# Kernel optimization log

Hardware: AMD Instinct MI355X
Metric: run time of the kernel (lower is better)

## Reference

```python
import jax, jax.numpy as jnp
import numpy as np

DIM = 4096
N_HEADS = 32
N_KV_HEADS = 8
HEAD_DIM = 128
B, S = 2, 2048


def setup_inputs() -> dict:
    key = jax.random.key(0)
    k1, k2, k3, k4, k5 = jax.random.split(key, 5)
    sc = 0.02
    return {
        "x": jax.random.normal(k1, (B, S, DIM), dtype=jnp.float32),
        "wq": jax.random.normal(k2, (N_HEADS * HEAD_DIM, DIM), dtype=jnp.float32) * sc,
        "wk": jax.random.normal(k3, (N_KV_HEADS * HEAD_DIM, DIM), dtype=jnp.float32) * sc,
        "wv": jax.random.normal(k4, (N_KV_HEADS * HEAD_DIM, DIM), dtype=jnp.float32) * sc,
        "wo": jax.random.normal(k5, (DIM, N_HEADS * HEAD_DIM), dtype=jnp.float32) * sc,
    }


def reference(x, wq, wk, wv, wo):
    b, s, _ = x.shape
    groups = N_HEADS // N_KV_HEADS
    # projections (torch Linear: y = x @ W.T)
    q = (x @ wq.T).reshape(b, s, N_HEADS, HEAD_DIM).transpose(0, 2, 1, 3)      # [b,H,s,d]
    k = (x @ wk.T).reshape(b, s, N_KV_HEADS, HEAD_DIM).transpose(0, 2, 1, 3)   # [b,Hkv,s,d]
    v = (x @ wv.T).reshape(b, s, N_KV_HEADS, HEAD_DIM).transpose(0, 2, 1, 3)
    # GQA: attend q grouped per kv head without materializing expanded k/v
    qg = q.reshape(b, N_KV_HEADS, groups, s, HEAD_DIM)                          # [b,Hkv,g,s,d]
    scores = jnp.einsum("bhgqd,bhkd->bhgqk", qg, k) * (HEAD_DIM ** -0.5)
    attn = jax.nn.softmax(scores, axis=-1)                                      # no causal mask (as in source)
    out = jnp.einsum("bhgqk,bhkd->bhgqd", attn, v)                              # [b,Hkv,g,s,d]
    out = out.reshape(b, N_HEADS, s, HEAD_DIM).transpose(0, 2, 1, 3).reshape(b, s, N_HEADS * HEAD_DIM)
    return out @ wo.T
```

## Files before the change

kernel.cpp:

```cpp
#include <hip/hip_runtime.h>
#include <stdint.h>


typedef __attribute__((ext_vector_type(4))) float f32x4;
typedef __attribute__((ext_vector_type(16))) float f32x16;
typedef __attribute__((ext_vector_type(4))) float float4v;
typedef __attribute__((ext_vector_type(8))) short short8;
typedef __attribute__((ext_vector_type(8))) __bf16 bf16x8;
typedef __attribute__((ext_vector_type(4))) unsigned short ushort4v;
typedef __attribute__((ext_vector_type(4))) unsigned int uint4v;

#define B_SZ 2
#define S_SZ 2048
#define DIM_SZ 4096
#define NH 32
#define NKV 8
#define HD 128
#define CEXP 0.12752531f

static __device__ __forceinline__ unsigned short f2bf(float f) {
  unsigned int u = __builtin_bit_cast(unsigned int, f);
  u = (u + 0x7fffu + ((u >> 16) & 1u)) >> 16;
  return (unsigned short)u;
}
static __device__ __forceinline__ f32x4 mfma16(short8 a, short8 b, f32x4 c) {
  return __builtin_amdgcn_mfma_f32_16x16x32_bf16(
      __builtin_bit_cast(bf16x8, a), __builtin_bit_cast(bf16x8, b), c, 0, 0, 0);
}
static __device__ __forceinline__ f32x16 mfma32(short8 a, short8 b, f32x16 c) {
  return __builtin_amdgcn_mfma_f32_32x32x16_bf16(
      __builtin_bit_cast(bf16x8, a), __builtin_bit_cast(bf16x8, b), c, 0, 0, 0);
}
static __device__ __forceinline__ void gload16(const void* g, void* l) {
  __builtin_amdgcn_global_load_lds(
      (const __attribute__((address_space(1))) unsigned int*)g,
      (__attribute__((address_space(3))) unsigned int*)l, 16, 0, 0);
}
static __device__ __forceinline__ unsigned int cvtpk(float lo, float hi) {
  unsigned int r;
  asm("v_cvt_pk_bf16_f32 %0, %1, %2" : "=v"(r) : "v"(lo), "v"(hi));
  return r;
}

__global__ __launch_bounds__(256) void cvt_kernel(const float* __restrict__ src,
                                                  unsigned short* __restrict__ dst,
                                                  int n4) {
  int i = blockIdx.x * 256 + threadIdx.x;
  if (i >= n4) return;
  float4v v = ((const float4v*)src)[i];
  ushort4v o;
  o[0] = f2bf(v[0]); o[1] = f2bf(v[1]); o[2] = f2bf(v[2]); o[3] = f2bf(v[3]);
  ((ushort4v*)dst)[i] = o;
}

template <int EPI>
__global__ __launch_bounds__(512, 2) void gemm256(const unsigned short* __restrict__ A,
                                                  const unsigned short* __restrict__ B,
                                                  void* __restrict__ Cout,
                                                  int N, int K, int H) {
  __shared__ unsigned short lds[65536];
  const int tid = threadIdx.x;
  const int lane = tid & 63;
  const int wave = tid >> 6;
  const int wm = wave >> 2;
  const int wn = wave & 3;
  const int fr = lane & 15, fg = lane >> 4;
  const int m0 = blockIdx.y * 256, n0 = blockIdx.x * 256;
  const int NT = K >> 6;

  auto seg = [&](int buf, int ab, int half) -> unsigned short* {
    return lds + ((((buf << 1) | ab) << 1) | half) * 8192;
  };

  const int srow = tid >> 3;
  const int scol = ((tid & 7) ^ (srow & 7)) << 3;
  const unsigned short* Abase = A + (size_t)(m0 + srow) * K + scol;
  const unsigned short* Bbase = B + (size_t)(n0 + srow) * K + scol;

  auto stageA = [&](int t, int h) {
    const unsigned short* g = Abase + (size_t)(h * 128) * K + t * 64;
    unsigned short* d = seg(t & 1, 0, h);
    gload16(g, d + tid * 8);
    gload16(g + (size_t)64 * K, d + 4096 + tid * 8);
  };
  auto stageB = [&](int t, int h) {
    const unsigned short* g = Bbase + (size_t)(h * 128) * K + t * 64;
    unsigned short* d = seg(t & 1, 1, h);
    gload16(g, d + tid * 8);
    gload16(g + (size_t)64 * K, d + 4096 + tid * 8);
  };

  f32x4 acc[8][4] = {};

  stageA(0, 0); stageA(0, 1);
  stageB(0, 0); stageB(0, 1);
  stageB(1, 0); stageB(1, 1);
  asm volatile("s_waitcnt vmcnt(4)" ::: "memory");
  __builtin_amdgcn_s_barrier();

#pragma unroll 1
  for (int t = 0; t < NT; ++t) {
    const unsigned short* Aseg = seg(t & 1, 0, wm);
    const unsigned short* Bseg = seg(t & 1, 1, wn >> 1);
    const int brow0 = (wn & 1) * 64;
    short8 aR[4][2], b01[2][2], b23[2][2];

#pragma unroll
    for (int mi = 0; mi < 4; ++mi)
#pragma unroll
      for (int ks = 0; ks < 2; ++ks) {
        const int row = mi * 16 + fr;
        aR[mi][ks] = *(const short8*)&Aseg[row * 64 + ((((ks << 2) + fg) ^ (row & 7)) << 3)];
      }
#pragma unroll
    for (int ni = 0; ni < 2; ++ni)
#pragma unroll
      for (int ks = 0; ks < 2; ++ks) {
        const int row = brow0 + ni * 16 + fr;
        b01[ni][ks] = *(const short8*)&Bseg[row * 64 + ((((ks << 2) + fg) ^ (row & 7)) << 3)];
      }
    if (t + 1 < NT) stageA(t + 1, 0);
    __builtin_amdgcn_sched_barrier(0);
    __builtin_amdgcn_s_barrier();
    asm volatile("s_waitcnt lgkmcnt(0)" ::: "memory");
    __builtin_amdgcn_sched_barrier(0);
    __builtin_amdgcn_s_setprio(1);
#pragma unroll
    for (int mi = 0; mi < 4; ++mi)
#pragma unroll
      for (int ni = 0; ni < 2; ++ni)
#pragma unroll
        for (int ks = 0; ks < 2; ++ks)
          acc[mi][ni] = mfma16(aR[mi][ks], b01[ni][ks], acc[mi][ni]);
    __builtin_amdgcn_s_setprio(0);
    __builtin_amdgcn_sched_barrier(0);
    __builtin_amdgcn_s_barrier();

#pragma unroll
    for (int ni = 0; ni < 2; ++ni)
#pragma unroll
      for (int ks = 0; ks < 2; ++ks) {
        const int row = brow0 + (ni + 2) * 16 + fr;
        b23[ni][ks] = *(const short8*)&Bseg[row * 64 + ((((ks << 2) + fg) ^ (row & 7)) << 3)];
      }
    if (t + 1 < NT) stageA(t + 1, 1);
    __builtin_amdgcn_sched_barrier(0);
    __builtin_amdgcn_s_barrier();
    asm volatile("s_waitcnt lgkmcnt(0)" ::: "memory");
    __builtin_amdgcn_sched_barrier(0);
    __builtin_amdgcn_s_setprio(1);
#pragma unroll
    for (int mi = 0; mi < 4; ++mi)
#pragma unroll
      for (int ni = 0; ni < 2; ++ni)
#pragma unroll
        for (int ks = 0; ks < 2; ++ks)
          acc[mi][ni + 2] = mfma16(aR[mi][ks], b23[ni][ks], acc[mi][ni + 2]);
    __builtin_amdgcn_s_setprio(0);
    __builtin_amdgcn_sched_barrier(0);
    __builtin_amdgcn_s_barrier();

#pragma unroll
    for (int mi = 0; mi < 4; ++mi)
#pragma unroll
      for (int ks = 0; ks < 2; ++ks) {
        const int row = (mi + 4) * 16 + fr;
        aR[mi][ks] = *(const short8*)&Aseg[row * 64 + ((((ks << 2) + fg) ^ (row & 7)) << 3)];
      }
    if (t + 2 < NT) stageB(t + 2, 0);
    __builtin_amdgcn_sched_barrier(0);
    __builtin_amdgcn_s_barrier();
    asm volatile("s_waitcnt lgkmcnt(0)" ::: "memory");
    __builtin_amdgcn_sched_barrier(0);
    __builtin_amdgcn_s_setprio(1);
#pragma unroll
    for (int mi = 0; mi < 4; ++mi)
#pragma unroll
      for (int ni = 0; ni < 2; ++ni)
#pragma unroll
        for (int ks = 0; ks < 2; ++ks)
          acc[mi + 4][ni] = mfma16(aR[mi][ks], b01[ni][ks], acc[mi + 4][ni]);
    __builtin_amdgcn_s_setprio(0);
    __builtin_amdgcn_sched_barrier(0);
    __builtin_amdgcn_s_barrier();

    if (t + 2 < NT) {
      stageB(t + 2, 1);
      __builtin_amdgcn_sched_barrier(0);
      asm volatile("s_waitcnt vmcnt(4)" ::: "memory");
    } else {
      __builtin_amdgcn_sched_barrier(0);
      asm volatile("s_waitcnt vmcnt(0)" ::: "memory");
    }
    __builtin_amdgcn_s_barrier();
    __builtin_amdgcn_s_setprio(1);
#pragma unroll
    for (int mi = 0; mi < 4; ++mi)
#pragma unroll
      for (int ni = 0; ni < 2; ++ni)
#pragma unroll
        for (int ks = 0; ks < 2; ++ks)
          acc[mi + 4][ni + 2] = mfma16(aR[mi][ks], b23[ni][ks], acc[mi + 4][ni + 2]);
    __builtin_amdgcn_s_setprio(0);
    __builtin_amdgcn_sched_barrier(0);
    __builtin_amdgcn_s_barrier();
  }

#pragma unroll
  for (int mi = 0; mi < 8; ++mi) {
#pragma unroll
    for (int ni = 0; ni < 4; ++ni) {
      const int mb = m0 + wm * 128 + mi * 16 + fg * 4;
      const int n = n0 + wn * 64 + ni * 16 + fr;
      if (EPI == 0) {
        float* C = (float*)Cout;
#pragma unroll
        for (int r = 0; r < 4; ++r) C[(size_t)(mb + r) * N + n] = acc[mi][ni][r];
      } else {
        unsigned short* C = (unsigned short*)Cout;
        const int h = n >> 7, d = n & 127;
#pragma unroll
        for (int r = 0; r < 4; ++r) {
          const int m = mb + r;
          const int bb = m >> 11, s = m & 2047;
          C[(((size_t)(bb * H + h)) * S_SZ + s) * HD + d] = f2bf(acc[mi][ni][r]);
        }
      }
    }
  }
}

template <int EPI>
__global__ __launch_bounds__(256) void gemm_bt(const unsigned short* __restrict__ A,
                                               const unsigned short* __restrict__ B,
                                               void* __restrict__ Cout,
                                               void* __restrict__ Cout2,
                                               int N, int K, int H) {
  __shared__ unsigned short As[128 * 32];
  __shared__ unsigned short Bs[128 * 32];
  const int tid = threadIdx.x;
  const int lane = tid & 63;
  const int wave = tid >> 6;
  const int wr = wave >> 1, wc = wave & 1;
  const int m0 = blockIdx.y * 128, n0 = blockIdx.x * 128;

  f32x4 acc[4][4] = {};

  const int srow = tid >> 2;
  const int swz8 = ((tid & 3) ^ (srow & 3)) * 8;
  const unsigned short* Ap0 = A + (size_t)(m0 + srow) * K + swz8;
  const unsigned short* Ap1 = Ap0 + (size_t)64 * K;
  const unsigned short* Bp0 = B + (size_t)(n0 + srow) * K + swz8;
  const unsigned short* Bp1 = Bp0 + (size_t)64 * K;
  unsigned short* Ad0 = As + tid * 8;
  unsigned short* Ad1 = As + 2048 + tid * 8;
  unsigned short* Bd0 = Bs + tid * 8;
  unsigned short* Bd1 = Bs + 2048 + tid * 8;

  const int fr = lane & 15;
  const int fg = lane >> 4;
  const int rsl = (fg ^ (fr & 3)) * 8;

#pragma unroll 1
  for (int kt = 0; kt < K; kt += 32) {
    gload16(Ap0 + kt, Ad0);
    gload16(Ap1 + kt, Ad1);
    gload16(Bp0 + kt, Bd0);
    gload16(Bp1 + kt, Bd1);
    __syncthreads();
    short8 a[4], b[4];
#pragma unroll
    for (int i = 0; i < 4; i++)
      a[i] = *(const short8*)&As[(wr * 64 + i * 16 + fr) * 32 + rsl];
#pragma unroll
    for (int i = 0; i < 4; i++)
      b[i] = *(const short8*)&Bs[(wc * 64 + i * 16 + fr) * 32 + rsl];
#pragma unroll
    for (int mi = 0; mi < 4; mi++)
#pragma unroll
      for (int ni = 0; ni < 4; ni++)
        acc[mi][ni] = mfma16(a[mi], b[ni], acc[mi][ni]);
    __syncthreads();
  }

#pragma unroll
  for (int mi = 0; mi < 4; mi++) {
#pragma unroll
    for (int ni = 0; ni < 4; ni++) {
      const int mb = m0 + wr * 64 + mi * 16 + fg * 4;
      const int n = n0 + wc * 64 + ni * 16 + fr;
      if (EPI == 0) {
        float* C = (float*)Cout;
#pragma unroll
        for (int r = 0; r < 4; r++) C[(size_t)(mb + r) * N + n] = acc[mi][ni][r];
      } else if (EPI == 3) {
        if (n < 1024) {
          unsigned short* C = (unsigned short*)Cout;
          const int h = n >> 7, d = n & 127;
#pragma unroll
          for (int r = 0; r < 4; r++) {
            const int m = mb + r;
            const int bb = m >> 11, s = m & 2047;
            C[(((size_t)(bb * NKV + h)) * S_SZ + s) * HD + d] = f2bf(acc[mi][ni][r]);
          }
        } else {
          unsigned short* C = (unsigned short*)Cout2;
          const int vr = n - 1024;
          const int h = vr >> 7, d = vr & 127;
          const int bb = mb >> 11, s = mb & 2047;
          ushort4v pk;
#pragma unroll
          for (int r = 0; r < 4; r++) pk[r] = f2bf(acc[mi][ni][r]);
          *(ushort4v*)&C[(((size_t)(bb * NKV + h)) * HD + d) * S_SZ + s] = pk;
        }
      }
    }
  }
}

__global__ __launch_bounds__(512) void attn_kernel(const unsigned short* __restrict__ Q,
                                                   const unsigned short* __restrict__ Kg,
                                                   const unsigned short* __restrict__ Vt,
                                                   unsigned short* __restrict__ AO) {
  __shared__ unsigned short Ks[2][64 * 128];
  __shared__ unsigned short Vs[2][128 * 64];
  const int tid = threadIdx.x, lane = tid & 63, w = tid >> 6;
  const int l31 = lane & 31, h = lane >> 5;
  const int qt = blockIdx.x, hq = blockIdx.y, b = blockIdx.z;
  const int hk = hq >> 2;
  const size_t qbase = ((size_t)(b * NH + hq) * S_SZ) * HD;
  const size_t kbase = ((size_t)(b * NKV + hk) * S_SZ) * HD;
  const size_t vbase = ((size_t)(b * NKV + hk) * HD) * S_SZ;
  const int q = qt * 256 + w * 32 + l31;

  short8 qf[8];
#pragma unroll
  for (int c = 0; c < 8; ++c)
    qf[c] = *(const short8*)&Q[qbase + (size_t)q * HD + c * 16 + h * 8];

  const int p0 = tid, p1 = tid + 512;
  const int kr0 = p0 >> 4, kc0 = ((p0 & 15) ^ (kr0 & 7)) << 3;
  const int kr1 = p1 >> 4, kc1 = ((p1 & 15) ^ (kr1 & 7)) << 3;
  const int vr0 = p0 >> 3, vc0 = ((p0 & 7) ^ (vr0 & 7)) << 3;
  const int vr1 = p1 >> 3, vc1 = ((p1 & 7) ^ (vr1 & 7)) << 3;

  auto stage = [&](int bufi, int kt) {
    gload16(&Kg[kbase + (size_t)(kt + kr0) * HD + kc0], &Ks[bufi][p0 * 8]);
    gload16(&Kg[kbase + (size_t)(kt + kr1) * HD + kc1], &Ks[bufi][p1 * 8]);
    gload16(&Vt[vbase + (size_t)vr0 * S_SZ + kt + vc0], &Vs[bufi][p0 * 8]);
    gload16(&Vt[vbase + (size_t)vr1 * S_SZ + kt + vc1], &Vs[bufi][p1 * 8]);
  };

  f32x16 ao[4] = {};
  float m_r = -3.0e38f, l_r = 0.f;

  stage(0, 0);
  asm volatile("s_waitcnt vmcnt(0)" ::: "memory");
  __syncthreads();

#pragma unroll 1
  for (int t = 0; t < 32; ++t) {
    const int cur = t & 1;
    if (t + 1 < 32) stage(cur ^ 1, (t + 1) * 64);
    const unsigned short* K_ = Ks[cur];
    const unsigned short* V_ = Vs[cur];

    f32x16 sf[2] = {};
#pragma unroll
    for (int kb = 0; kb < 2; ++kb) {
      const int row = kb * 32 + l31;
#pragma unroll
      for (int c = 0; c < 8; ++c) {
        const int ch = (c * 2 + h) ^ (row & 7);
        short8 kf = *(const short8*)&K_[row * 128 + ch * 8];
        sf[kb] = mfma32(kf, qf[c], sf[kb]);
      }
    }

    float tm = sf[0][0];
#pragma unroll
    for (int r = 1; r < 16; ++r) tm = fmaxf(tm, sf[0][r]);
#pragma unroll
    for (int r = 0; r < 16; ++r) tm = fmaxf(tm, sf[1][r]);
    tm = fmaxf(tm, __shfl_xor(tm, 32));

    const bool skip = ((tm - m_r) * CEXP <= 8.0f);
    if (!__all(skip)) {
      const float mnew = fmaxf(m_r, tm);
      const float al = __builtin_amdgcn_exp2f((m_r - mnew) * CEXP);
      l_r *= al;
#pragma unroll
      for (int db = 0; db < 4; ++db)
#pragma unroll
        for (int r = 0; r < 16; ++r) ao[db][r] *= al;
      m_r = mnew;
    }

    const float nmc = -m_r * CEXP;
    float p[2][16];
    float ps = 0.f;
#pragma unroll
    for (int kb = 0; kb < 2; ++kb)
#pragma unroll
      for (int r = 0; r < 16; ++r) {
        p[kb][r] = __builtin_amdgcn_exp2f(fmaf(sf[kb][r], CEXP, nmc));
        ps += p[kb][r];
      }
    ps += __shfl_xor(ps, 32);
    l_r += ps;

    uint4v pw[4];
#pragma unroll
    for (int kb = 0; kb < 2; ++kb)
#pragma unroll
      for (int hs = 0; hs < 2; ++hs) {
        const int f = kb * 2 + hs;
        const unsigned int X  = cvtpk(p[kb][hs * 8 + 0], p[kb][hs * 8 + 1]);
        const unsigned int X2 = cvtpk(p[kb][hs * 8 + 2], p[kb][hs * 8 + 3]);
        const unsigned int Y  = cvtpk(p[kb][hs * 8 + 4], p[kb][hs * 8 + 5]);
        const unsigned int Y2 = cvtpk(p[kb][hs * 8 + 6], p[kb][hs * 8 + 7]);
        const unsigned int xs  = __shfl_xor(X, 32);
        const unsigned int xs2 = __shfl_xor(X2, 32);
        const unsigned int ys  = __shfl_xor(Y, 32);
        const unsigned int ys2 = __shfl_xor(Y2, 32);
        pw[f][0] = h ? ys : X;
        pw[f][1] = h ? ys2 : X2;
        pw[f][2] = h ? Y : xs;
        pw[f][3] = h ? Y2 : xs2;
      }

#pragma unroll
    for (int db = 0; db < 4; ++db) {
      const int row = db * 32 + l31;
#pragma unroll
      for (int f = 0; f < 4; ++f) {
        const int ch = (f * 2 + h) ^ (row & 7);
        short8 vf = *(const short8*)&V_[row * 64 + ch * 8];
        ao[db] = mfma32(vf, __builtin_bit_cast(short8, pw[f]), ao[db]);
      }
    }

    asm volatile("s_waitcnt vmcnt(0)" ::: "memory");
    __syncthreads();
  }

  const float inv = 1.0f / l_r;
  const size_t ob = (((size_t)(b * S_SZ + q)) * NH + hq) * HD;
#pragma unroll
  for (int db = 0; db < 4; ++db)
#pragma unroll
    for (int rg = 0; rg < 4; ++rg) {
      const int d0 = db * 32 + rg * 8 + h * 4;
      ushort4v pk;
#pragma unroll
      for (int j = 0; j < 4; ++j) pk[j] = f2bf(ao[db][rg * 4 + j] * inv);
      *(ushort4v*)&AO[ob + d0] = pk;
    }
}

extern "C" void kernel_launch(void* const* d_in, const int* in_sizes, int n_in,
                              void* d_out, int out_size, void* d_ws, size_t ws_size,
                              hipStream_t stream) {
  const float* x  = (const float*)d_in[0];
  const float* wq = (const float*)d_in[1];
  const float* wk = (const float*)d_in[2];
  const float* wv = (const float*)d_in[3];
  const float* wo = (const float*)d_in[4];

  unsigned short* ws = (unsigned short*)d_ws;
  const size_t SZ_BIG = (size_t)DIM_SZ * DIM_SZ;
  const size_t SZ_SMALL = (size_t)(NKV * HD) * DIM_SZ;
  unsigned short* xb   = ws;
  unsigned short* wbig = xb + SZ_BIG;
  unsigned short* wkb  = wbig + SZ_BIG;
  unsigned short* wvb  = wkb + SZ_SMALL;
  unsigned short* Qb   = wvb + SZ_SMALL;
  unsigned short* Kb   = Qb + SZ_BIG;
  unsigned short* Vtb  = Kb + SZ_SMALL;
  unsigned short* AOb  = Vtb + SZ_SMALL;

  cvt_kernel<<<16384, 256, 0, stream>>>(x, xb, 4194304);
  cvt_kernel<<<16384, 256, 0, stream>>>(wq, wbig, 4194304);
  cvt_kernel<<<4096, 256, 0, stream>>>(wk, wkb, 1048576);
  cvt_kernel<<<4096, 256, 0, stream>>>(wv, wvb, 1048576);

  gemm256<1><<<dim3(16, 16), 512, 0, stream>>>(xb, wbig, Qb, 4096, DIM_SZ, NH);
  gemm_bt<3><<<dim3(16, 32), 256, 0, stream>>>(xb, wkb, Kb, Vtb, 2048, DIM_SZ, NKV);

  attn_kernel<<<dim3(8, 32, 2), 512, 0, stream>>>(Qb, Kb, Vtb, AOb);

  cvt_kernel<<<16384, 256, 0, stream>>>(wo, wbig, 4194304);
  gemm256<0><<<dim3(16, 16), 512, 0, stream>>>(AOb, wbig, d_out, 4096, DIM_SZ, NH);
}
```

Baseline: 744.2 us.

## Use permlane32 swaps in attention and swizzle GEMM workgroup order

Replaces the ds_bpermute-based cross-half-wave shuffles in the attention softmax (max, sum, and the P fragment repacking) with v_permlane32_swap, which exchanges the two 32-lane halves without going through LDS. Separately, both GEMM kernels remap the linear block index so that consecutive blocks are spread in strides across the grid, aiming for better L2/MALL locality across XCDs. The remap assumes the block count is divisible by 8.

```diff
diff --git a/kernel.cpp b/kernel.cpp
--- a/kernel.cpp
+++ b/kernel.cpp
@@ -9,6 +9,7 @@
 typedef __attribute__((ext_vector_type(8))) __bf16 bf16x8;
 typedef __attribute__((ext_vector_type(4))) unsigned short ushort4v;
 typedef __attribute__((ext_vector_type(4))) unsigned int uint4v;
+typedef __attribute__((ext_vector_type(2))) unsigned int uint2v;
 
 #define B_SZ 2
 #define S_SZ 2048
@@ -40,6 +41,14 @@
   unsigned int r;
   asm("v_cvt_pk_bf16_f32 %0, %1, %2" : "=v"(r) : "v"(lo), "v"(hi));
   return r;
+}
+static __device__ __forceinline__ uint2v plswap(unsigned int a, unsigned int b) {
+  return __builtin_amdgcn_permlane32_swap(a, b, false, false);
+}
+static __device__ __forceinline__ float halfswap(float x, int h) {
+  const unsigned int u = __builtin_bit_cast(unsigned int, x);
+  uint2v r = plswap(u, u);
+  return __builtin_bit_cast(float, h ? r[0] : r[1]);
 }
 
 __global__ __launch_bounds__(256) void cvt_kernel(const float* __restrict__ src,
@@ -65,7 +74,10 @@
   const int wm = wave >> 2;
   const int wn = wave & 3;
   const int fr = lane & 15, fg = lane >> 4;
-  const int m0 = blockIdx.y * 256, n0 = blockIdx.x * 256;
+  const int nwg = gridDim.x * gridDim.y;
+  int lin = blockIdx.y * gridDim.x + blockIdx.x;
+  lin = (lin & 7) * (nwg >> 3) + (lin >> 3);
+  const int m0 = (lin / gridDim.x) * 256, n0 = (lin % gridDim.x) * 256;
   const int NT = K >> 6;
 
   auto seg = [&](int buf, int ab, int half) -> unsigned short* {
@@ -242,7 +254,10 @@
   const int lane = tid & 63;
   const int wave = tid >> 6;
   const int wr = wave >> 1, wc = wave & 1;
-  const int m0 = blockIdx.y * 128, n0 = blockIdx.x * 128;
+  const int nwg = gridDim.x * gridDim.y;
+  int lin = blockIdx.y * gridDim.x + blockIdx.x;
+  lin = (lin & 7) * (nwg >> 3) + (lin >> 3);
+  const int m0 = (lin / gridDim.x) * 128, n0 = (lin % gridDim.x) * 128;
 
   f32x4 acc[4][4] = {};
 
@@ -382,7 +397,7 @@
     for (int r = 1; r < 16; ++r) tm = fmaxf(tm, sf[0][r]);
 #pragma unroll
     for (int r = 0; r < 16; ++r) tm = fmaxf(tm, sf[1][r]);
-    tm = fmaxf(tm, __shfl_xor(tm, 32));
+    tm = fmaxf(tm, halfswap(tm, h));
 
     const bool skip = ((tm - m_r) * CEXP <= 8.0f);
     if (!__all(skip)) {
@@ -406,7 +421,7 @@
         p[kb][r] = __builtin_amdgcn_exp2f(fmaf(sf[kb][r], CEXP, nmc));
         ps += p[kb][r];
       }
-    ps += __shfl_xor(ps, 32);
+    ps += halfswap(ps, h);
     l_r += ps;
 
     uint4v pw[4];
@@ -415,18 +430,13 @@
 #pragma unroll
       for (int hs = 0; hs < 2; ++hs) {
         const int f = kb * 2 + hs;
-        const unsigned int X  = cvtpk(p[kb][hs * 8 + 0], p[kb][hs * 8 + 1]);
+        const unsigned int X1 = cvtpk(p[kb][hs * 8 + 0], p[kb][hs * 8 + 1]);
+        const unsigned int Y1 = cvtpk(p[kb][hs * 8 + 4], p[kb][hs * 8 + 5]);
         const unsigned int X2 = cvtpk(p[kb][hs * 8 + 2], p[kb][hs * 8 + 3]);
-        const unsigned int Y  = cvtpk(p[kb][hs * 8 + 4], p[kb][hs * 8 + 5]);
         const unsigned int Y2 = cvtpk(p[kb][hs * 8 + 6], p[kb][hs * 8 + 7]);
-        const unsigned int xs  = __shfl_xor(X, 32);
-        const unsigned int xs2 = __shfl_xor(X2, 32);
-        const unsigned int ys  = __shfl_xor(Y, 32);
-        const unsigned int ys2 = __shfl_xor(Y2, 32);
-        pw[f][0] = h ? ys : X;
-        pw[f][1] = h ? ys2 : X2;
-        pw[f][2] = h ? Y : xs;
-        pw[f][3] = h ? Y2 : xs2;
+        uint2v s1 = plswap(X1, Y1);
+        uint2v s2 = plswap(X2, Y2);
+        pw[f][0] = s1[0]; pw[f][1] = s2[0]; pw[f][2] = s1[1]; pw[f][3] = s2[1];
       }
 
 #pragma unroll
```

After: 720.1 us. 3.2% less time.
